# Kernel optimization log

Hardware: AMD Instinct MI355X
Metric: run time of the kernel (lower is better)

Reference implementation:

```python
import jax, jax.numpy as jnp
import numpy as np

NB_RADIUSES = 24
SIGMA = 0.1


def setup_inputs() -> dict:
    key = jax.random.key(0)
    k1, k2, k3 = jax.random.split(key, 3)
    nb, nf, nx, ny, nz = 2, 2, 256, 256, 16
    x = jax.random.uniform(k1, (nb, nf, nx, ny, nz), dtype=jnp.float32)
    # center of mass: real part is the column coordinate (in [0, ny)),
    # imag part is the row coordinate (in [0, nx)) -- keep centers inside the plane
    com_real = jax.random.uniform(k2, (nb, nf, nz), dtype=jnp.float32) * ny
    com_imag = jax.random.uniform(k3, (nb, nf, nz), dtype=jnp.float32) * nx
    return {"x": x, "com_real": com_real, "com_imag": com_imag}


def reference(x, com_real, com_imag):
    nb, nf, nx, ny, nz = x.shape
    # complex plan: real = index % ny (column), imag = index // ny (row)
    col = jnp.arange(ny, dtype=jnp.float32)   # real axis
    row = jnp.arange(nx, dtype=jnp.float32)   # imag axis
    # centered plan, broadcast to (nb, nf, nx, ny, nz)
    dx = col[None, None, None, :, None] - com_real[:, :, None, None, :]
    dy = row[None, None, :, None, None] - com_imag[:, :, None, None, :]
    theta = jnp.arctan2(dy, dx)           # arg(centered_plan)
    theta_neg = jnp.arctan2(-dy, -dx)     # arg(-centered_plan)

    # angles i*(2pi/nr) - pi; branch selection identical to the torch code
    angles = np.arange(NB_RADIUSES) * (2.0 * np.pi / NB_RADIUSES) - np.pi
    use_neg = (angles > 0.5 * np.pi) | (angles < -0.5 * np.pi)
    targets = np.where(angles > 0.5 * np.pi, angles - np.pi,
                       np.where(angles < -0.5 * np.pi, angles + np.pi, angles))
    use_neg = jnp.asarray(use_neg)
    targets = jnp.asarray(targets.astype(np.float32))

    # select angle field per radius: (R, nb, nf, nx, ny, nz)
    sel = jnp.where(use_neg[:, None, None, None, None, None],
                    theta_neg[None], theta[None])
    coef = jnp.float32(1.0 / (SIGMA * np.sqrt(2.0 * np.pi)))
    diff = sel - targets[:, None, None, None, None, None]
    w = coef * jnp.exp(-(diff ** 2) / jnp.float32(2.0 * SIGMA ** 2))

    # gaussian-weighted reduction over the (x, y) plane, keep z
    s = jnp.einsum('Rbfxyz,bfxyz->bfRz', w, x)
    return jnp.sqrt(2.0 * s)
```

## Files before the change

### kernel.cpp

```cpp
#include <hip/hip_runtime.h>

#define NR 24
#define NBATCH 2
#define NFEAT 2
#define NX 256
#define NY 256
#define NZ 16
#define PAD 25

__global__ __launch_bounds__(256) void grx_partial(
    const float* __restrict__ x,
    const float* __restrict__ com_real,
    const float* __restrict__ com_imag,
    float* __restrict__ ws)
{
    __shared__ float red[256 * PAD];

    const int tid  = threadIdx.x;
    const int z    = tid & 15;
    const int c0   = tid >> 4;
    const int half = blockIdx.x & 1;
    const int row  = (blockIdx.x >> 1) & (NX - 1);
    const int bf   = blockIdx.x >> 9;

    float* myred = &red[tid * PAD];
    #pragma unroll
    for (int i = 0; i < PAD; ++i) myred[i] = 0.0f;

    const float comr = com_real[bf * NZ + z];
    const float comi = com_imag[bf * NZ + z];
    const float dyv  = (float)row - comi;
    const float ady  = fabsf(dyv);

    const float PIF   = 3.14159265358979f;
    const float PI_2  = 1.57079632679490f;
    const float C_PSI = 3.81971863420549f;
    const float C_E   = -3.4269908169872414f;

    const float* xp = x + ((size_t)(bf * NX + row)) * (NY * NZ);

    #pragma unroll 2
    for (int kk = 0; kk < 8; ++kk) {
        const int col  = c0 + ((half * 8 + kk) << 4);
        const float xv = xp[col * NZ + z];
        const float dxv = (float)col - comr;

        const float adx = fabsf(dxv);
        const float mn  = fminf(adx, ady);
        const float mx  = fmaxf(adx, ady);
        const float t   = mn * __builtin_amdgcn_rcpf(fmaxf(mx, 1e-30f));
        const float r2  = t * t;
        float p = fmaf(r2, 0.0208351f, -0.0851330f);
        p = fmaf(r2, p, 0.1801410f);
        p = fmaf(r2, p, -0.3302995f);
        p = fmaf(r2, p, 0.9998660f);
        float th = t * p;
        if (ady > adx)  th = PI_2 - th;
        if (dxv < 0.0f) th = PIF - th;
        th = copysignf(th, dyv);

        const float psi = th * C_PSI;
        const float nf  = rintf(psi);
        const float f   = psi - nf;
        const int base  = (int)nf + 12;

        const float fm = f + 1.0f;
        const float fp = f - 1.0f;
        const float w0 = __expf(C_E * f  * f ) * xv;
        const float wm = __expf(C_E * fm * fm) * xv;
        const float wp = __expf(C_E * fp * fp) * xv;

        int v0 = base - 1; v0 = (v0 < 0)   ? v0 + 24 : v0;
        int v1 = base;     v1 = (v1 >= 24) ? v1 - 24 : v1;
        int v2 = base + 1; v2 = (v2 >= 24) ? v2 - 24 : v2;

        myred[v0] += wm;
        myred[v1] += w0;
        myred[v2] += wp;
    }

    __syncthreads();

    for (int o = tid; o < NR * NZ; o += 256) {
        const int r  = o >> 4;
        const int zz = o & 15;
        float s = 0.0f;
        #pragma unroll
        for (int c = 0; c < 16; ++c)
            s += red[(c * 16 + zz) * PAD + r];
        atomicAdd(&ws[(bf * NR + r) * NZ + zz], s);
    }
}

__global__ void grx_finalize(const float* __restrict__ ws, float* __restrict__ out, int n)
{
    const int i = blockIdx.x * blockDim.x + threadIdx.x;
    if (i < n) {
        const float coef = 3.9894228040143270f;
        out[i] = sqrtf(2.0f * coef * ws[i]);
    }
}

extern "C" void kernel_launch(void* const* d_in, const int* in_sizes, int n_in,
                              void* d_out, int out_size, void* d_ws, size_t ws_size,
                              hipStream_t stream)
{
    const float* x  = (const float*)d_in[0];
    const float* cr = (const float*)d_in[1];
    const float* ci = (const float*)d_in[2];
    float* out = (float*)d_out;
    float* ws  = (float*)d_ws;

    const int nout = NBATCH * NFEAT * NR * NZ;
    (void)hipMemsetAsync(ws, 0, nout * sizeof(float), stream);

    grx_partial<<<dim3(NBATCH * NFEAT * NX * 2), dim3(256), 0, stream>>>(x, cr, ci, ws);
    grx_finalize<<<dim3((nout + 255) / 256), dim3(256), 0, stream>>>(ws, out, nout);
}
```

Before: 90.06 us.

## Replace global atomics with per-block partials and a separate reduction kernel

Each partial block now writes its 384 sums to its own slot in the workspace instead of atomically adding into a shared output buffer, and a new reduce kernel sums the 512 partials per output with wave shuffles before applying sqrt. This removes atomic contention (512 blocks hitting the same 384 addresses per batch-feature) and the memset launch. In exchange it writes and reads about 3 MB of partials, and the reduce kernel's reads are strided by NPART floats, so they are poorly coalesced.

```diff
diff --git a/kernel.cpp b/kernel.cpp
--- a/kernel.cpp
+++ b/kernel.cpp
@@ -7,6 +7,8 @@
 #define NY 256
 #define NZ 16
 #define PAD 25
+#define NBLK_PER_BF 512
+#define NPART (NR * NZ)
 
 __global__ __launch_bounds__(256) void grx_partial(
     const float* __restrict__ x,
@@ -81,23 +83,39 @@
 
     __syncthreads();
 
-    for (int o = tid; o < NR * NZ; o += 256) {
+    float* wsb = ws + (size_t)blockIdx.x * NPART;
+    for (int o = tid; o < NPART; o += 256) {
         const int r  = o >> 4;
         const int zz = o & 15;
         float s = 0.0f;
         #pragma unroll
         for (int c = 0; c < 16; ++c)
             s += red[(c * 16 + zz) * PAD + r];
-        atomicAdd(&ws[(bf * NR + r) * NZ + zz], s);
+        wsb[o] = s;
     }
 }
 
-__global__ void grx_finalize(const float* __restrict__ ws, float* __restrict__ out, int n)
+__global__ __launch_bounds__(256) void grx_reduce(
+    const float* __restrict__ ws, float* __restrict__ out)
 {
-    const int i = blockIdx.x * blockDim.x + threadIdx.x;
-    if (i < n) {
+    const int b  = blockIdx.x;
+    const int bf = b / NPART;
+    const int o  = b - bf * NPART;
+    const int tid = threadIdx.x;
+
+    const float* base = ws + (size_t)bf * NBLK_PER_BF * NPART + o;
+    float s = base[(size_t)tid * NPART] + base[(size_t)(tid + 256) * NPART];
+
+    #pragma unroll
+    for (int off = 32; off; off >>= 1) s += __shfl_down(s, off, 64);
+
+    __shared__ float w4[4];
+    if ((tid & 63) == 0) w4[tid >> 6] = s;
+    __syncthreads();
+    if (tid == 0) {
         const float coef = 3.9894228040143270f;
-        out[i] = sqrtf(2.0f * coef * ws[i]);
+        const float tot = w4[0] + w4[1] + w4[2] + w4[3];
+        out[b] = sqrtf(2.0f * coef * tot);
     }
 }
 
@@ -111,9 +129,6 @@
     float* out = (float*)d_out;
     float* ws  = (float*)d_ws;
 
-    const int nout = NBATCH * NFEAT * NR * NZ;
-    (void)hipMemsetAsync(ws, 0, nout * sizeof(float), stream);
-
-    grx_partial<<<dim3(NBATCH * NFEAT * NX * 2), dim3(256), 0, stream>>>(x, cr, ci, ws);
-    grx_finalize<<<dim3((nout + 255) / 256), dim3(256), 0, stream>>>(ws, out, nout);
+    grx_partial<<<dim3(NBATCH * NFEAT * NBLK_PER_BF), dim3(256), 0, stream>>>(x, cr, ci, ws);
+    grx_reduce<<<dim3(NBATCH * NFEAT * NPART), dim3(256), 0, stream>>>(ws, out);
 }
```

New measurement: 78.83 us. 12.5% less time.
